# Kernel tuning notes

Measured on AMD Instinct MI355X. Metric: run time of the kernel, lower is better.

## Reference

```python
import jax, jax.numpy as jnp
import numpy as np

N, E, C = 50000, 300000, 256  # nodes, edges, hidden size


def setup_inputs() -> dict:
    key = jax.random.key(0)
    ks = jax.random.split(key, 12)
    s = 0.05  # param init scale
    return {
        "x": jax.random.normal(ks[0], (N, C), dtype=jnp.float32),
        "edge_index": jax.random.randint(ks[1], (2, E), 0, N, dtype=jnp.int32),
        # GATConv layer 1 (heads=1): shared lin weight, att_src/att_dst vectors, bias
        "W1": jax.random.normal(ks[2], (C, C), dtype=jnp.float32) * s,
        "a1_src": jax.random.normal(ks[3], (C,), dtype=jnp.float32) * s,
        "a1_dst": jax.random.normal(ks[4], (C,), dtype=jnp.float32) * s,
        "b1": jnp.zeros((C,), dtype=jnp.float32),
        # GATConv layer 2
        "W2": jax.random.normal(ks[5], (C, C), dtype=jnp.float32) * s,
        "a2_src": jax.random.normal(ks[6], (C,), dtype=jnp.float32) * s,
        "a2_dst": jax.random.normal(ks[7], (C,), dtype=jnp.float32) * s,
        "b2": jnp.zeros((C,), dtype=jnp.float32),
        # Final Linear (torch convention: W [out, in], y = x @ W.T + b)
        "Wl": jax.random.normal(ks[8], (C, C), dtype=jnp.float32) * s,
        "bl": jnp.zeros((C,), dtype=jnp.float32),
    }


def _gat_conv(x, src, dst, W, a_src, a_dst, b):
    # PyG GATConv, heads=1, negative_slope=0.2, self-loops already appended.
    h = x @ W                                  # [N, C]
    alpha_src = h @ a_src                      # [N]
    alpha_dst = h @ a_dst                      # [N]
    e = jax.nn.leaky_relu(alpha_src[src] + alpha_dst[dst], 0.2)   # [E']
    # numerically stable softmax over incoming edges of each destination node
    m = jax.ops.segment_max(e, dst, num_segments=N)               # [N]
    ex = jnp.exp(e - m[dst])
    den = jax.ops.segment_sum(ex, dst, num_segments=N)            # [N]
    w = ex / den[dst]                                              # [E']
    out = jax.ops.segment_sum(h[src] * w[:, None], dst, num_segments=N)  # [N, C]
    return out + b


def reference(x, edge_index, W1, a1_src, a1_dst, b1, W2, a2_src, a2_dst, b2, Wl, bl):
    # add_self_loops (done inside each GATConv in PyG; appending once to the
    # input edge list is equivalent since both convs see the same edges)
    loops = jnp.arange(N, dtype=edge_index.dtype)
    ei = jnp.concatenate([edge_index, jnp.stack([loops, loops])], axis=1)
    src, dst = ei[0], ei[1]
    x = jax.nn.relu(_gat_conv(x, src, dst, W1, a1_src, a1_dst, b1))
    x = jax.nn.relu(_gat_conv(x, src, dst, W2, a2_src, a2_dst, b2))
    return x @ Wl.T + bl
```

## Files before the change

kernel.cpp:

```cpp
#include <hip/hip_runtime.h>

#define NN 50000
#define EE 300000
#define ET (EE + NN)
#define CD 256
#define PAD_M 50176
#define NB 196

typedef unsigned short ushortT;
typedef short bf16x8 __attribute__((ext_vector_type(8)));
typedef float f32x4 __attribute__((ext_vector_type(4)));

__device__ __forceinline__ ushortT f2b(float f) {
    unsigned u = __builtin_bit_cast(unsigned, f);
    unsigned r = (u + 0x7FFFu + ((u >> 16) & 1u)) >> 16;
    return (ushortT)r;
}
__device__ __forceinline__ float b2f(ushortT b) {
    return __builtin_bit_cast(float, ((unsigned)b) << 16);
}

#define PREP_X 12500
#define PREP_W1 12564
#define PREP_W2 12628
#define PREP_WL 12692
#define PREP_END 12888

__global__ __launch_bounds__(256) void prep_kernel(
    const float* __restrict__ x, const float* __restrict__ W1,
    const float* __restrict__ W2, const float* __restrict__ Wl,
    ushortT* __restrict__ B0, ushortT* __restrict__ W1t,
    ushortT* __restrict__ W2t, ushortT* __restrict__ Wlt,
    int* __restrict__ deg, float* __restrict__ asA, float* __restrict__ adA,
    float* __restrict__ asB, float* __restrict__ adB) {
    __shared__ float t[32][33];
    int b = blockIdx.x, tidx = threadIdx.x;
    if (b < PREP_X) {
        int id = b * 256 + tidx;
        float4 v = *(const float4*)(x + (size_t)id * 4);
        ushort4 o;
        o.x = f2b(v.x); o.y = f2b(v.y); o.z = f2b(v.z); o.w = f2b(v.w);
        *(ushort4*)(B0 + (size_t)id * 4) = o;
    } else if (b < PREP_W2) {
        const float* W = (b < PREP_W1) ? W1 : W2;
        ushortT* Bt = (b < PREP_W1) ? W1t : W2t;
        int rel = b - ((b < PREP_W1) ? PREP_X : PREP_W1);
        int bx = (rel & 7) * 32;
        int by = (rel >> 3) * 32;
        int xx = tidx & 31, yy = tidx >> 5;
        for (int y = yy; y < 32; y += 8) t[y][xx] = W[(size_t)(bx + y) * CD + by + xx];
        __syncthreads();
        for (int y = yy; y < 32; y += 8)
            Bt[(size_t)(by + y) * CD + bx + xx] = f2b(t[xx][y]);
    } else if (b < PREP_WL) {
        int id = (b - PREP_W2) * 256 + tidx;
        float4 v = *(const float4*)(Wl + (size_t)id * 4);
        ushort4 o;
        o.x = f2b(v.x); o.y = f2b(v.y); o.z = f2b(v.z); o.w = f2b(v.w);
        *(ushort4*)(Wlt + (size_t)id * 4) = o;
    } else {
        int i = (b - PREP_WL) * 256 + tidx;
        if (i < NN) {
            deg[i] = 1;
            asA[i] = 0.f; adA[i] = 0.f;
            asB[i] = 0.f; adB[i] = 0.f;
        }
    }
}


__global__ void count_deg_kernel(const int* __restrict__ ei, int* __restrict__ deg) {
    int i = blockIdx.x * blockDim.x + threadIdx.x;
    if (i < EE) atomicAdd(&deg[ei[EE + i]], 1);
}

__global__ __launch_bounds__(256) void scan_part(const int* __restrict__ deg,
                                                 int* __restrict__ bsum) {
    int i = blockIdx.x * 256 + threadIdx.x;
    int v = (i < NN) ? deg[i] : 0;
#pragma unroll
    for (int off = 32; off > 0; off >>= 1) v += __shfl_down(v, off);
    __shared__ int w[4];
    if ((threadIdx.x & 63) == 0) w[threadIdx.x >> 6] = v;
    __syncthreads();
    if (threadIdx.x == 0) bsum[blockIdx.x] = w[0] + w[1] + w[2] + w[3];
}

__global__ __launch_bounds__(256) void scan_top(const int* __restrict__ bsum,
                                                int* __restrict__ boffs,
                                                int* __restrict__ row_start) {
    __shared__ int s[256];
    int t = threadIdx.x;
    int v = (t < NB) ? bsum[t] : 0;
    s[t] = v;
    __syncthreads();
    for (int off = 1; off < 256; off <<= 1) {
        int x = s[t];
        int y = (t >= off) ? s[t - off] : 0;
        __syncthreads();
        s[t] = x + y;
        __syncthreads();
    }
    if (t < NB) boffs[t] = s[t] - v;
    if (t == 0) row_start[NN] = ET;
}

__global__ __launch_bounds__(256) void scan_fill(const int* __restrict__ deg,
                                                 const int* __restrict__ boffs,
                                                 int* __restrict__ row_start,
                                                 int* __restrict__ fill_pos) {
    __shared__ int s[256];
    int t = threadIdx.x;
    int i = blockIdx.x * 256 + t;
    int v = (i < NN) ? deg[i] : 0;
    s[t] = v;
    __syncthreads();
    for (int off = 1; off < 256; off <<= 1) {
        int x = s[t];
        int y = (t >= off) ? s[t - off] : 0;
        __syncthreads();
        s[t] = x + y;
        __syncthreads();
    }
    int excl = s[t] - v + boffs[blockIdx.x];
    if (i < NN) {
        row_start[i] = excl;
        fill_pos[i] = excl;
    }
}

__global__ void fill_csr_kernel(const int* __restrict__ ei, int* __restrict__ fill_pos,
                                int* __restrict__ srcs) {
    int i = blockIdx.x * blockDim.x + threadIdx.x;
    if (i < EE) {
        int s = ei[i];
        int d = ei[EE + i];
        int p = atomicAdd(&fill_pos[d], 1);
        srcs[p] = s;
    } else if (i < ET) {
        int n = i - EE;
        int p = atomicAdd(&fill_pos[n], 1);
        srcs[p] = n;
    }
}


template <int OUTF32, int ALPHA>
__global__ __launch_bounds__(256, 4) void gemm_mfma(const ushortT* __restrict__ A,
                                                    const ushortT* __restrict__ Bt,
                                                    const float* __restrict__ bias,
                                                    float* __restrict__ outF,
                                                    ushortT* __restrict__ outB,
                                                    const float* __restrict__ a_src,
                                                    const float* __restrict__ a_dst,
                                                    float* __restrict__ as_g,
                                                    float* __restrict__ ad_g,
                                                    int M) {
    __shared__ ushortT Bs[64 * 256];
    int tid = threadIdx.x;
    int wave = tid >> 6, lane = tid & 63;
    int wm = wave * 32;
    int bm = blockIdx.x * 128, bn = blockIdx.y * 64;
    int l15 = lane & 15, quad = lane >> 4;

#pragma unroll
    for (int p = 0; p < 8; ++p) {
        int c = p * 256 + tid;
        int slot = c >> 5;
        int piece = c & 31;
        int col = (slot & 15) * 4 + (slot >> 4);
        int spiece = piece ^ (slot & 31);
        const ushortT* gb = Bt + (size_t)(bn + col) * CD + spiece * 8;
        __builtin_amdgcn_global_load_lds(
            (const __attribute__((address_space(1))) void*)gb,
            (__attribute__((address_space(3))) void*)(Bs + (size_t)(p * 256 + wave * 64) * 8),
            16, 0, 0);
    }
    __syncthreads();

    f32x4 acc[2][4] = {};

#pragma unroll
    for (int kk = 0; kk < 8; ++kk) {
        bf16x8 a[2], b[4];
#pragma unroll
        for (int i = 0; i < 2; ++i)
            a[i] = *(const bf16x8*)(A + (size_t)(bm + wm + i * 16 + l15) * CD + kk * 32 + quad * 8);
        int kc = kk * 4 + quad;
#pragma unroll
        for (int j = 0; j < 4; ++j) {
            int slot = j * 16 + l15;
            b[j] = *(const bf16x8*)(Bs + (size_t)slot * 256 + (size_t)(kc ^ (slot & 31)) * 8);
        }
#pragma unroll
        for (int i = 0; i < 2; ++i)
#pragma unroll
            for (int j = 0; j < 4; ++j)
                acc[i][j] = __builtin_amdgcn_mfma_f32_16x16x32_bf16(a[i], b[j], acc[i][j], 0, 0, 0);
    }

    int colb = bn + l15 * 4;
#pragma unroll
    for (int i = 0; i < 2; ++i) {
#pragma unroll
        for (int r = 0; r < 4; ++r) {
            int row = bm + wm + i * 16 + quad * 4 + r;
            if (OUTF32) {
                if (row < M) {
                    float4 bv = *(const float4*)(bias + colb);
                    float4 v;
                    v.x = acc[i][0][r] + bv.x;
                    v.y = acc[i][1][r] + bv.y;
                    v.z = acc[i][2][r] + bv.z;
                    v.w = acc[i][3][r] + bv.w;
                    *(float4*)(outF + (size_t)row * CD + colb) = v;
                }
            } else {
                ushort4 o;
                o.x = f2b(acc[i][0][r]);
                o.y = f2b(acc[i][1][r]);
                o.z = f2b(acc[i][2][r]);
                o.w = f2b(acc[i][3][r]);
                *(ushort4*)(outB + (size_t)row * CD + colb) = o;
            }
        }
    }

    if (ALPHA) {
        float4 avs = *(const float4*)(a_src + colb);
        float4 avd = *(const float4*)(a_dst + colb);
#pragma unroll
        for (int i = 0; i < 2; ++i) {
#pragma unroll
            for (int r = 0; r < 4; ++r) {
                int row = bm + wm + i * 16 + quad * 4 + r;
                float ps = acc[i][0][r] * avs.x + acc[i][1][r] * avs.y +
                           acc[i][2][r] * avs.z + acc[i][3][r] * avs.w;
                float pd = acc[i][0][r] * avd.x + acc[i][1][r] * avd.y +
                           acc[i][2][r] * avd.z + acc[i][3][r] * avd.w;
#pragma unroll
                for (int off = 1; off < 16; off <<= 1) {
                    ps += __shfl_xor(ps, off);
                    pd += __shfl_xor(pd, off);
                }
                if (l15 == 0 && row < M) {
                    atomicAdd(&as_g[row], ps);
                    atomicAdd(&ad_g[row], pd);
                }
            }
        }
    }
}


__device__ __forceinline__ float lrelu02(float x) { return x > 0.f ? x : 0.2f * x; }

__global__ __launch_bounds__(256) void gat_agg(const ushortT* __restrict__ h,
                                               const float* __restrict__ as_,
                                               const float* __restrict__ ad_,
                                               const int* __restrict__ row_start,
                                               const int* __restrict__ srcs,
                                               const float* __restrict__ bias,
                                               ushortT* __restrict__ out) {
    int node = blockIdx.x * 4 + (threadIdx.x >> 6);
    int lane = threadIdx.x & 63;
    if (node >= NN) return;
    int rs = row_start[node];
    int re = row_start[node + 1];
    int deg = re - rs;
    float adst = ad_[node];

    float a0 = 0.f, a1 = 0.f, a2 = 0.f, a3 = 0.f;

    if (deg <= 64) {
        int s_lane = srcs[rs + ((lane < deg) ? lane : 0)];
        float e = (lane < deg) ? lrelu02(as_[s_lane] + adst) : -1e30f;
        float m = e;
#pragma unroll
        for (int off = 1; off < 64; off <<= 1) m = fmaxf(m, __shfl_xor(m, off));
        float ex = (lane < deg) ? __expf(e - m) : 0.f;
        float den = ex;
#pragma unroll
        for (int off = 1; off < 64; off <<= 1) den += __shfl_xor(den, off);
        float wl = ex / den;

        for (int kk = 0; kk < deg; kk += 8) {
            int s[8];
            float w[8];
#pragma unroll
            for (int t = 0; t < 8; ++t) {
                int idx = kk + t;
                int ii = (idx < deg) ? idx : kk;
                int sv = __shfl(s_lane, ii);
                float wv = __shfl(wl, ii);
                s[t] = sv;
                w[t] = (idx < deg) ? wv : 0.f;
            }
            ushort4 hv[8];
#pragma unroll
            for (int t = 0; t < 8; ++t)
                hv[t] = *(const ushort4*)(h + (size_t)s[t] * CD + lane * 4);
#pragma unroll
            for (int t = 0; t < 8; ++t) {
                a0 += w[t] * b2f(hv[t].x);
                a1 += w[t] * b2f(hv[t].y);
                a2 += w[t] * b2f(hv[t].z);
                a3 += w[t] * b2f(hv[t].w);
            }
        }
    } else {
        float m = -1e30f;
        for (int k = rs + lane; k < re; k += 64) {
            float e = lrelu02(as_[srcs[k]] + adst);
            m = fmaxf(m, e);
        }
#pragma unroll
        for (int off = 1; off < 64; off <<= 1) m = fmaxf(m, __shfl_xor(m, off));
        float den = 0.f;
        for (int k = rs + lane; k < re; k += 64) {
            float e = lrelu02(as_[srcs[k]] + adst);
            den += __expf(e - m);
        }
#pragma unroll
        for (int off = 1; off < 64; off <<= 1) den += __shfl_xor(den, off);
        float inv_den = 1.f / den;
        for (int k = rs; k < re; ++k) {
            int s = srcs[k];
            float e = lrelu02(as_[s] + adst);
            float w = __expf(e - m) * inv_den;
            ushort4 hv = *(const ushort4*)(h + (size_t)s * CD + lane * 4);
            a0 += w * b2f(hv.x);
            a1 += w * b2f(hv.y);
            a2 += w * b2f(hv.z);
            a3 += w * b2f(hv.w);
        }
    }

    float4 b4 = *(const float4*)(bias + lane * 4);
    a0 = fmaxf(a0 + b4.x, 0.f);
    a1 = fmaxf(a1 + b4.y, 0.f);
    a2 = fmaxf(a2 + b4.z, 0.f);
    a3 = fmaxf(a3 + b4.w, 0.f);
    ushort4 o;
    o.x = f2b(a0);
    o.y = f2b(a1);
    o.z = f2b(a2);
    o.w = f2b(a3);
    *(ushort4*)(out + (size_t)node * CD + lane * 4) = o;
}


extern "C" void kernel_launch(void* const* d_in, const int* in_sizes, int n_in,
                              void* d_out, int out_size, void* d_ws, size_t ws_size,
                              hipStream_t stream) {
    const float* x = (const float*)d_in[0];
    const int* ei = (const int*)d_in[1];
    const float* W1 = (const float*)d_in[2];
    const float* a1s = (const float*)d_in[3];
    const float* a1d = (const float*)d_in[4];
    const float* b1 = (const float*)d_in[5];
    const float* W2 = (const float*)d_in[6];
    const float* a2s = (const float*)d_in[7];
    const float* a2d = (const float*)d_in[8];
    const float* b2 = (const float*)d_in[9];
    const float* Wl = (const float*)d_in[10];
    const float* bl = (const float*)d_in[11];
    float* out = (float*)d_out;

    char* w = (char*)d_ws;
    ushortT* B0 = (ushortT*)w; w += (size_t)PAD_M * CD * 2;
    ushortT* B1 = (ushortT*)w; w += (size_t)PAD_M * CD * 2;
    ushortT* B2 = (ushortT*)w; w += (size_t)PAD_M * CD * 2;
    ushortT* W1t = (ushortT*)w; w += (size_t)CD * CD * 2;
    ushortT* W2t = (ushortT*)w; w += (size_t)CD * CD * 2;
    ushortT* Wlt = (ushortT*)w; w += (size_t)CD * CD * 2;
    float* asA = (float*)w; w += (size_t)NN * 4;
    float* adA = (float*)w; w += (size_t)NN * 4;
    float* asB = (float*)w; w += (size_t)NN * 4;
    float* adB = (float*)w; w += (size_t)NN * 4;
    int* deg = (int*)w; w += (size_t)NN * 4;
    int* fill_pos = (int*)w; w += (size_t)NN * 4;
    int* srcs = (int*)w; w += (size_t)ET * 4;
    int* bsum = (int*)w; w += 1024;
    int* boffs = (int*)w; w += 1024;
    int* row_start = (int*)w; w += (size_t)(NN + 1) * 4;

    prep_kernel<<<PREP_END, 256, 0, stream>>>(x, W1, W2, Wl, B0, W1t, W2t, Wlt,
                                              deg, asA, adA, asB, adB);

    count_deg_kernel<<<(EE + 255) / 256, 256, 0, stream>>>(ei, deg);
    scan_part<<<NB, 256, 0, stream>>>(deg, bsum);
    scan_top<<<1, 256, 0, stream>>>(bsum, boffs, row_start);
    scan_fill<<<NB, 256, 0, stream>>>(deg, boffs, row_start, fill_pos);
    fill_csr_kernel<<<(ET + 255) / 256, 256, 0, stream>>>(ei, fill_pos, srcs);

    dim3 ggrid(PAD_M / 128, 4);
    int nwave_blocks = (NN + 3) / 4;

    gemm_mfma<0, 1><<<ggrid, 256, 0, stream>>>(B0, W1t, nullptr, nullptr, B1,
                                               a1s, a1d, asA, adA, NN);
    gat_agg<<<nwave_blocks, 256, 0, stream>>>(B1, asA, adA, row_start, srcs, b1, B2);

    gemm_mfma<0, 1><<<ggrid, 256, 0, stream>>>(B2, W2t, nullptr, nullptr, B1,
                                               a2s, a2d, asB, adB, NN);
    gat_agg<<<nwave_blocks, 256, 0, stream>>>(B1, asB, adB, row_start, srcs, b2, B0);

    gemm_mfma<1, 0><<<ggrid, 256, 0, stream>>>(B0, Wlt, bl, out, nullptr,
                                               nullptr, nullptr, nullptr, nullptr, NN);
}
```

Before: 295.5 us.

## Fuse scan_top into scan_fill, prefetch A tiles, and linearize GEMM grid

Removes the single-block scan_top launch by having every scan_fill block redundantly scan the 196 block sums itself, which drops one kernel launch and its serialization. In the GEMM, all A fragments for the full K dimension are loaded into registers before the barrier so they overlap with the async LDS load of B. The 2D grid is flattened so the four N-tiles of the same row block are adjacent, improving A reuse in cache. Holding A in registers raises register pressure and may reduce occupancy.

```diff
diff --git a/kernel.cpp b/kernel.cpp
--- a/kernel.cpp
+++ b/kernel.cpp
@@ -86,13 +86,14 @@
     if (threadIdx.x == 0) bsum[blockIdx.x] = w[0] + w[1] + w[2] + w[3];
 }
 
-__global__ __launch_bounds__(256) void scan_top(const int* __restrict__ bsum,
-                                                int* __restrict__ boffs,
-                                                int* __restrict__ row_start) {
+__global__ __launch_bounds__(256) void scan_fill(const int* __restrict__ deg,
+                                                 const int* __restrict__ bsum,
+                                                 int* __restrict__ row_start,
+                                                 int* __restrict__ fill_pos) {
     __shared__ int s[256];
     int t = threadIdx.x;
-    int v = (t < NB) ? bsum[t] : 0;
-    s[t] = v;
+    int bv = (t < NB) ? bsum[t] : 0;
+    s[t] = bv;
     __syncthreads();
     for (int off = 1; off < 256; off <<= 1) {
         int x = s[t];
@@ -101,16 +102,8 @@
         s[t] = x + y;
         __syncthreads();
     }
-    if (t < NB) boffs[t] = s[t] - v;
-    if (t == 0) row_start[NN] = ET;
-}
-
-__global__ __launch_bounds__(256) void scan_fill(const int* __restrict__ deg,
-                                                 const int* __restrict__ boffs,
-                                                 int* __restrict__ row_start,
-                                                 int* __restrict__ fill_pos) {
-    __shared__ int s[256];
-    int t = threadIdx.x;
+    int boff = s[blockIdx.x] - bsum[blockIdx.x];
+    __syncthreads();
     int i = blockIdx.x * 256 + t;
     int v = (i < NN) ? deg[i] : 0;
     s[t] = v;
@@ -122,11 +115,12 @@
         s[t] = x + y;
         __syncthreads();
     }
-    int excl = s[t] - v + boffs[blockIdx.x];
+    int excl = s[t] - v + boff;
     if (i < NN) {
         row_start[i] = excl;
         fill_pos[i] = excl;
     }
+    if (blockIdx.x == 0 && t == 0) row_start[NN] = ET;
 }
 
 __global__ void fill_csr_kernel(const int* __restrict__ ei, int* __restrict__ fill_pos,
@@ -160,7 +154,8 @@
     int tid = threadIdx.x;
     int wave = tid >> 6, lane = tid & 63;
     int wm = wave * 32;
-    int bm = blockIdx.x * 128, bn = blockIdx.y * 64;
+    int id = blockIdx.x;
+    int bm = (id >> 2) * 128, bn = (id & 3) * 64;
     int l15 = lane & 15, quad = lane >> 4;
 
 #pragma unroll
@@ -176,16 +171,21 @@
             (__attribute__((address_space(3))) void*)(Bs + (size_t)(p * 256 + wave * 64) * 8),
             16, 0, 0);
     }
+
+    bf16x8 a[2][8];
+#pragma unroll
+    for (int kk = 0; kk < 8; ++kk)
+#pragma unroll
+        for (int i = 0; i < 2; ++i)
+            a[i][kk] = *(const bf16x8*)(A + (size_t)(bm + wm + i * 16 + l15) * CD + kk * 32 + quad * 8);
+
     __syncthreads();
 
     f32x4 acc[2][4] = {};
 
 #pragma unroll
     for (int kk = 0; kk < 8; ++kk) {
-        bf16x8 a[2], b[4];
-#pragma unroll
-        for (int i = 0; i < 2; ++i)
-            a[i] = *(const bf16x8*)(A + (size_t)(bm + wm + i * 16 + l15) * CD + kk * 32 + quad * 8);
+        bf16x8 b[4];
         int kc = kk * 4 + quad;
 #pragma unroll
         for (int j = 0; j < 4; ++j) {
@@ -196,7 +196,7 @@
         for (int i = 0; i < 2; ++i)
 #pragma unroll
             for (int j = 0; j < 4; ++j)
-                acc[i][j] = __builtin_amdgcn_mfma_f32_16x16x32_bf16(a[i], b[j], acc[i][j], 0, 0, 0);
+                acc[i][j] = __builtin_amdgcn_mfma_f32_16x16x32_bf16(a[i][kk], b[j], acc[i][j], 0, 0, 0);
     }
 
     int colb = bn + l15 * 4;
@@ -382,7 +382,6 @@
     int* fill_pos = (int*)w; w += (size_t)NN * 4;
     int* srcs = (int*)w; w += (size_t)ET * 4;
     int* bsum = (int*)w; w += 1024;
-    int* boffs = (int*)w; w += 1024;
     int* row_start = (int*)w; w += (size_t)(NN + 1) * 4;
 
     prep_kernel<<<PREP_END, 256, 0, stream>>>(x, W1, W2, Wl, B0, W1t, W2t, Wlt,
@@ -390,11 +389,10 @@
 
     count_deg_kernel<<<(EE + 255) / 256, 256, 0, stream>>>(ei, deg);
     scan_part<<<NB, 256, 0, stream>>>(deg, bsum);
-    scan_top<<<1, 256, 0, stream>>>(bsum, boffs, row_start);
-    scan_fill<<<NB, 256, 0, stream>>>(deg, boffs, row_start, fill_pos);
+    scan_fill<<<NB, 256, 0, stream>>>(deg, bsum, row_start, fill_pos);
     fill_csr_kernel<<<(ET + 255) / 256, 256, 0, stream>>>(ei, fill_pos, srcs);
 
-    dim3 ggrid(PAD_M / 128, 4);
+    int ggrid = (PAD_M / 128) * 4;
     int nwave_blocks = (NN + 3) / 4;
 
     gemm_mfma<0, 1><<<ggrid, 256, 0, stream>>>(B0, W1t, nullptr, nullptr, B1,
```

Result: no change. 295.1 us (-0.1%).
